# Performance work log

Hardware: AMD Instinct MI355X
Metric: run time of the kernel (lower is better)

Reference implementation:

```python
import jax, jax.numpy as jnp
import numpy as np

N = 50000   # nodes
E = 640000  # edges
IN_C, HID_C, OUT_C = 128, 128, 64


def _glorot(key, shape):
    lim = float(np.sqrt(6.0 / (shape[0] + shape[1])))
    return jax.random.uniform(key, shape, jnp.float32, -lim, lim)


def setup_inputs() -> dict:
    key = jax.random.key(0)
    ks = jax.random.split(key, 6)
    x = jax.random.normal(ks[0], (N, IN_C), jnp.float32)
    edge_index = jax.random.randint(ks[1], (2, E), 0, N, dtype=jnp.int64)
    W1 = _glorot(ks[2], (IN_C, HID_C));  b1 = jnp.zeros((HID_C,), jnp.float32)
    W2 = _glorot(ks[3], (HID_C, HID_C)); b2 = jnp.zeros((HID_C,), jnp.float32)
    W3 = _glorot(ks[4], (HID_C, OUT_C)); b3 = jnp.zeros((OUT_C,), jnp.float32)
    return {"x": x, "edge_index": edge_index,
            "W1": W1, "b1": b1, "W2": W2, "b2": b2, "W3": W3, "b3": b3}


def gcn_conv(x, W, b, src, dst, n_nodes):
    """PyG GCNConv (eval): add self-loops, D^-1/2 (A+I) D^-1/2, linear, bias."""
    h = x @ W  # [N, out]
    ones = jnp.ones(src.shape[0], h.dtype)
    # degree including the self-loop (+1 per node)
    deg = jax.ops.segment_sum(ones, dst, num_segments=n_nodes) + 1.0
    dinv_sqrt = jax.lax.rsqrt(deg)
    coef = dinv_sqrt[src] * dinv_sqrt[dst]               # [E]
    agg = jax.ops.segment_sum(h[src] * coef[:, None], dst, num_segments=n_nodes)
    agg = agg + h * (1.0 / deg)[:, None]                 # self-loop term: 1/deg[i]
    return agg + b


def reference(x, edge_index, W1, b1, W2, b2, W3, b3):
    src, dst = edge_index[0], edge_index[1]
    h = jax.nn.relu(gcn_conv(x, W1, b1, src, dst, N))
    h = jax.nn.relu(gcn_conv(h, W2, b2, src, dst, N))
    return gcn_conv(h, W3, b3, src, dst, N)
```

## Files before the change

kernel.cpp:

```cpp
#include <hip/hip_runtime.h>


#define K_DIM 128
#define POISON 0xAAAAAAAAu

typedef __attribute__((ext_vector_type(8))) short bf16x8;
typedef __attribute__((ext_vector_type(4))) float f32x4;

__device__ __forceinline__ unsigned short f2bf(float x) {
    unsigned u = __float_as_uint(x);
    return (unsigned short)((u + 0x7fffu + ((u >> 16) & 1u)) >> 16);
}
__device__ __forceinline__ float bflo(unsigned v) { return __uint_as_float(v << 16); }
__device__ __forceinline__ float bfhi(unsigned v) { return __uint_as_float(v & 0xffff0000u); }

__device__ __forceinline__ void add8(float* acc, uint4 v) {
    acc[0] += bflo(v.x); acc[1] += bfhi(v.x);
    acc[2] += bflo(v.y); acc[3] += bfhi(v.y);
    acc[4] += bflo(v.z); acc[5] += bfhi(v.z);
    acc[6] += bflo(v.w); acc[7] += bfhi(v.w);
}

template <int COUT>
__device__ __forceinline__ void gemm_tile_f32(const float* __restrict__ X,
                                              const unsigned short* __restrict__ Wt,
                                              const float* __restrict__ rsd,
                                              unsigned short* __restrict__ Hb,
                                              int nrows, int tile, int tid) {
    constexpr int NT = COUT / 16;
    const int wave = tid >> 6;
    const int lane = tid & 63;
    const int m16 = lane & 15;
    const int kg  = lane >> 4;
    const int r0w = tile * 64 + wave * 16;

    int arow = r0w + m16;
    if (arow >= nrows) arow = nrows - 1;

    bf16x8 a[4];
#pragma unroll
    for (int kb = 0; kb < 4; ++kb) {
        const float* xp = &X[(size_t)arow * 128 + kb * 32 + kg * 8];
        float4 v0 = *(const float4*)xp;
        float4 v1 = *(const float4*)(xp + 4);
        union { bf16x8 v; unsigned short u[8]; } ua;
        ua.u[0] = f2bf(v0.x); ua.u[1] = f2bf(v0.y);
        ua.u[2] = f2bf(v0.z); ua.u[3] = f2bf(v0.w);
        ua.u[4] = f2bf(v1.x); ua.u[5] = f2bf(v1.y);
        ua.u[6] = f2bf(v1.z); ua.u[7] = f2bf(v1.w);
        a[kb] = ua.v;
    }

    f32x4 acc[NT];
#pragma unroll
    for (int t = 0; t < NT; ++t) acc[t] = (f32x4){0.f, 0.f, 0.f, 0.f};

#pragma unroll
    for (int t = 0; t < NT; ++t) {
        const unsigned short* wp = &Wt[(size_t)(t * 16 + m16) * 128 + kg * 8];
#pragma unroll
        for (int kb = 0; kb < 4; ++kb) {
            bf16x8 b = *(const bf16x8*)&wp[kb * 32];
            acc[t] = __builtin_amdgcn_mfma_f32_16x16x32_bf16(a[kb], b, acc[t], 0, 0, 0);
        }
    }

    const int rowb = r0w + kg * 4;
#pragma unroll
    for (int t = 0; t < NT; ++t) {
#pragma unroll
        for (int i = 0; i < 4; ++i) {
            int r = rowb + i;
            if (r < nrows)
                Hb[(size_t)r * COUT + t * 16 + m16] = f2bf(acc[t][i] * rsd[r]);
        }
    }
}

__global__ void k_count_cvt(const int* __restrict__ dst, int* __restrict__ cnt,
                            unsigned short* __restrict__ erank,
                            const float* __restrict__ W1, const float* __restrict__ W2,
                            const float* __restrict__ W3,
                            unsigned short* __restrict__ Wt1, unsigned short* __restrict__ Wt2,
                            unsigned short* __restrict__ Wt3,
                            int E, int gCount) {
    if ((int)blockIdx.x < gCount) {
        const int G = gCount * 256;
        const int g = blockIdx.x * 256 + threadIdx.x;
        int d[4], ev[4];
#pragma unroll
        for (int q = 0; q < 4; ++q) {
            int e = g + q * G;
            ev[q] = e;
            d[q] = (e < E) ? dst[e] : -1;
        }
#pragma unroll
        for (int q = 0; q < 4; ++q)
            if (d[q] >= 0) {
                unsigned old = (unsigned)atomicAdd(&cnt[d[q]], 1);
                erank[ev[q]] = (unsigned short)(old - POISON);
            }
        return;
    }
    int j = (blockIdx.x - gCount) * 256 + threadIdx.x;
    if (j < 16384) { int nn = j >> 7, k = j & 127; Wt1[nn * 128 + k] = f2bf(W1[k * 128 + nn]); return; }
    j -= 16384;
    if (j < 16384) { int nn = j >> 7, k = j & 127; Wt2[nn * 128 + k] = f2bf(W2[k * 128 + nn]); return; }
    j -= 16384;
    if (j < 8192)  { int nn = j >> 7, k = j & 127; Wt3[nn * 128 + k] = f2bf(W3[k * 64 + nn]); return; }
}

__global__ void k_scan_block(const int* __restrict__ cnt, int* __restrict__ rowptr,
                             int* __restrict__ bsum, float* __restrict__ rsd, int n) {
    __shared__ int s[256];
    int t = threadIdx.x;
    int i = blockIdx.x * 256 + t;
    int v = (i < n) ? (int)((unsigned)cnt[i] - POISON) : 0;
    if (i < n) rsd[i] = rsqrtf((float)v + 1.0f);
    s[t] = v;
    __syncthreads();
#pragma unroll
    for (int d = 1; d < 256; d <<= 1) {
        int u = (t >= d) ? s[t - d] : 0;
        __syncthreads();
        s[t] += u;
        __syncthreads();
    }
    if (i < n) rowptr[i] = s[t] - v;
    if (t == 255) bsum[blockIdx.x] = s[255];
}

__global__ void k_scan_add(const int* __restrict__ bsum, int* __restrict__ rowptr,
                           int n, int E, int nscan) {
    __shared__ int s[256];
    __shared__ int off;
    int t = threadIdx.x;
    int v = (t < nscan) ? bsum[t] : 0;
    s[t] = v;
    __syncthreads();
#pragma unroll
    for (int d = 1; d < 256; d <<= 1) {
        int u = (t >= d) ? s[t - d] : 0;
        __syncthreads();
        s[t] += u;
        __syncthreads();
    }
    if (t == (int)blockIdx.x) off = s[t] - v;
    __syncthreads();
    int i = blockIdx.x * 256 + t;
    if (i < n) rowptr[i] += off;
    if (i == 0) rowptr[n] = E;
}

__global__ __launch_bounds__(256)
void k_fill_gemm1(const int* __restrict__ src, const int* __restrict__ dst,
                  const unsigned short* __restrict__ erank,
                  const int* __restrict__ rowptr, int* __restrict__ col,
                  const float* __restrict__ x, const unsigned short* __restrict__ Wt1,
                  const float* __restrict__ rsd, unsigned short* __restrict__ Hb1,
                  int N, int E, int gFill) {
    if ((int)blockIdx.x < gFill) {
        const int G = gFill * 256;
        const int g = blockIdx.x * 256 + threadIdx.x;
        int d[4], sv[4], rk[4];
#pragma unroll
        for (int q = 0; q < 4; ++q) {
            int e = g + q * G;
            if (e < E) { d[q] = dst[e]; sv[q] = src[e]; rk[q] = erank[e]; }
            else d[q] = -1;
        }
        int base[4];
#pragma unroll
        for (int q = 0; q < 4; ++q)
            if (d[q] >= 0) base[q] = rowptr[d[q]];
#pragma unroll
        for (int q = 0; q < 4; ++q)
            if (d[q] >= 0) col[base[q] + rk[q]] = sv[q];
        return;
    }
    gemm_tile_f32<128>(x, Wt1, rsd, Hb1, N, blockIdx.x - gFill, threadIdx.x);
}

template <int COUT>
__launch_bounds__(256)
__global__ void k_agg_gemm(const unsigned short* __restrict__ Hin,
                           const int* __restrict__ rowptr, const int* __restrict__ col,
                           const float* __restrict__ rsd, const float* __restrict__ bias,
                           const unsigned short* __restrict__ Wt,
                           unsigned short* __restrict__ Hout, int n) {
    constexpr int NT = COUT / 32;
    __shared__ unsigned short As[32][136];
    const int tid = threadIdx.x;
    const int r0 = blockIdx.x * 32;

    {
        const int lr = tid >> 3;
        const int lc = (tid & 7) * 16;
        const int row = r0 + lr;
        const int rc = (row < n) ? row : (n - 1);

        float acc[16];
#pragma unroll
        for (int j = 0; j < 16; ++j) acc[j] = 0.0f;
        {
            const unsigned short* hp = &Hin[(size_t)rc * 128 + lc];
            add8(acc, *(const uint4*)hp);
            add8(acc + 8, *(const uint4*)(hp + 8));
        }
        int e = rowptr[rc], end = rowptr[rc + 1];
        for (; e + 3 < end; e += 4) {
            const unsigned short* p0 = &Hin[(size_t)col[e]     * 128 + lc];
            const unsigned short* p1 = &Hin[(size_t)col[e + 1] * 128 + lc];
            const unsigned short* p2 = &Hin[(size_t)col[e + 2] * 128 + lc];
            const unsigned short* p3 = &Hin[(size_t)col[e + 3] * 128 + lc];
            uint4 a0 = *(const uint4*)p0, a1 = *(const uint4*)(p0 + 8);
            uint4 b0 = *(const uint4*)p1, b1 = *(const uint4*)(p1 + 8);
            uint4 c0 = *(const uint4*)p2, c1 = *(const uint4*)(p2 + 8);
            uint4 d0 = *(const uint4*)p3, d1 = *(const uint4*)(p3 + 8);
            add8(acc, a0); add8(acc + 8, a1);
            add8(acc, b0); add8(acc + 8, b1);
            add8(acc, c0); add8(acc + 8, c1);
            add8(acc, d0); add8(acc + 8, d1);
        }
        for (; e < end; ++e) {
            const unsigned short* p0 = &Hin[(size_t)col[e] * 128 + lc];
            add8(acc, *(const uint4*)p0);
            add8(acc + 8, *(const uint4*)(p0 + 8));
        }

        const float rs = rsd[rc];
        float r[16];
#pragma unroll
        for (int q = 0; q < 4; ++q) {
            float4 bq = *(const float4*)&bias[lc + q * 4];
            r[q * 4 + 0] = fmaxf(bq.x + rs * acc[q * 4 + 0], 0.0f);
            r[q * 4 + 1] = fmaxf(bq.y + rs * acc[q * 4 + 1], 0.0f);
            r[q * 4 + 2] = fmaxf(bq.z + rs * acc[q * 4 + 2], 0.0f);
            r[q * 4 + 3] = fmaxf(bq.w + rs * acc[q * 4 + 3], 0.0f);
        }
        uint4 o0, o1;
        o0.x = (unsigned)f2bf(r[0])  | ((unsigned)f2bf(r[1])  << 16);
        o0.y = (unsigned)f2bf(r[2])  | ((unsigned)f2bf(r[3])  << 16);
        o0.z = (unsigned)f2bf(r[4])  | ((unsigned)f2bf(r[5])  << 16);
        o0.w = (unsigned)f2bf(r[6])  | ((unsigned)f2bf(r[7])  << 16);
        o1.x = (unsigned)f2bf(r[8])  | ((unsigned)f2bf(r[9])  << 16);
        o1.y = (unsigned)f2bf(r[10]) | ((unsigned)f2bf(r[11]) << 16);
        o1.z = (unsigned)f2bf(r[12]) | ((unsigned)f2bf(r[13]) << 16);
        o1.w = (unsigned)f2bf(r[14]) | ((unsigned)f2bf(r[15]) << 16);
        *(uint4*)&As[lr][lc] = o0;
        *(uint4*)&As[lr][lc + 8] = o1;
    }
    __syncthreads();

    const int wave = tid >> 6;
    const int lane = tid & 63;
    const int m16 = lane & 15;
    const int kg  = lane >> 4;
    const int rloc = (wave >> 1) * 16 + m16;
    const int cbase = (wave & 1) * (COUT / 2);

    bf16x8 a[4];
#pragma unroll
    for (int kb = 0; kb < 4; ++kb)
        a[kb] = *(const bf16x8*)&As[rloc][kb * 32 + kg * 8];

    f32x4 acc2[NT];
#pragma unroll
    for (int t = 0; t < NT; ++t) acc2[t] = (f32x4){0.f, 0.f, 0.f, 0.f};

#pragma unroll
    for (int t = 0; t < NT; ++t) {
        const unsigned short* wp = &Wt[(size_t)(cbase + t * 16 + m16) * 128 + kg * 8];
#pragma unroll
        for (int kb = 0; kb < 4; ++kb) {
            bf16x8 b = *(const bf16x8*)&wp[kb * 32];
            acc2[t] = __builtin_amdgcn_mfma_f32_16x16x32_bf16(a[kb], b, acc2[t], 0, 0, 0);
        }
    }

    const int rowb = r0 + (wave >> 1) * 16 + kg * 4;
#pragma unroll
    for (int t = 0; t < NT; ++t) {
#pragma unroll
        for (int i = 0; i < 4; ++i) {
            int r = rowb + i;
            if (r < n)
                Hout[(size_t)r * COUT + cbase + t * 16 + m16] = f2bf(acc2[t][i] * rsd[r]);
        }
    }
}

template <int C>
__launch_bounds__(256)
__global__ void k_agg_final(const unsigned short* __restrict__ Hb,
                            const int* __restrict__ rowptr, const int* __restrict__ col,
                            const float* __restrict__ rsd, const float* __restrict__ bias,
                            float* __restrict__ OUT, int n) {
    constexpr int TPN = C / 8;
    constexpr int NPB = 256 / TPN;
    const int node = blockIdx.x * NPB + threadIdx.x / TPN;
    const int c = (threadIdx.x % TPN) * 8;
    if (node >= n) return;

    float acc[8];
#pragma unroll
    for (int j = 0; j < 8; ++j) acc[j] = 0.0f;
    add8(acc, *(const uint4*)&Hb[(size_t)node * C + c]);

    int e = rowptr[node], end = rowptr[node + 1];
    for (; e + 3 < end; e += 4) {
        uint4 v0 = *(const uint4*)&Hb[(size_t)col[e]     * C + c];
        uint4 v1 = *(const uint4*)&Hb[(size_t)col[e + 1] * C + c];
        uint4 v2 = *(const uint4*)&Hb[(size_t)col[e + 2] * C + c];
        uint4 v3 = *(const uint4*)&Hb[(size_t)col[e + 3] * C + c];
        add8(acc, v0); add8(acc, v1); add8(acc, v2); add8(acc, v3);
    }
    for (; e < end; ++e)
        add8(acc, *(const uint4*)&Hb[(size_t)col[e] * C + c]);

    const float rs = rsd[node];
    const float4 b0 = *(const float4*)&bias[c];
    const float4 b1 = *(const float4*)&bias[c + 4];
    float* po = &OUT[(size_t)node * C + c];
    *(float4*)&po[0] = make_float4(b0.x + rs * acc[0], b0.y + rs * acc[1],
                                   b0.z + rs * acc[2], b0.w + rs * acc[3]);
    *(float4*)&po[4] = make_float4(b1.x + rs * acc[4], b1.y + rs * acc[5],
                                   b1.z + rs * acc[6], b1.w + rs * acc[7]);
}


extern "C" void kernel_launch(void* const* d_in, const int* in_sizes, int n_in,
                              void* d_out, int out_size, void* d_ws, size_t ws_size,
                              hipStream_t stream) {
    const float* x  = (const float*)d_in[0];
    const int*   ei = (const int*)d_in[1];
    const float* W1 = (const float*)d_in[2];
    const float* b1 = (const float*)d_in[3];
    const float* W2 = (const float*)d_in[4];
    const float* b2 = (const float*)d_in[5];
    const float* W3 = (const float*)d_in[6];
    const float* b3 = (const float*)d_in[7];

    const int N = in_sizes[0] / K_DIM;
    const int E = in_sizes[1] / 2;
    const int* srcv = ei;
    const int* dstv = ei + E;

    char* ws = (char*)d_ws;
    size_t off = 0;
    auto alloc = [&](size_t bytes) {
        char* p = ws + off;
        off += (bytes + 255) & ~(size_t)255;
        return p;
    };
    int*   cnt    = (int*)alloc((size_t)N * 4);
    int*   rowptr = (int*)alloc((size_t)(N + 1) * 4);
    int*   bsum   = (int*)alloc(256 * 4);
    float* rsd    = (float*)alloc((size_t)N * 4);
    int*   col    = (int*)alloc((size_t)E * 4);
    unsigned short* erank = (unsigned short*)alloc((size_t)E * 2);
    unsigned short* Wt1 = (unsigned short*)alloc(128 * 128 * 2);
    unsigned short* Wt2 = (unsigned short*)alloc(128 * 128 * 2);
    unsigned short* Wt3 = (unsigned short*)alloc(64 * 128 * 2);
    unsigned short* Hb1 = (unsigned short*)alloc((size_t)N * 128 * 2);
    unsigned short* Hb2 = (unsigned short*)alloc((size_t)N * 128 * 2);
    unsigned short* Hb3 = (unsigned short*)alloc((size_t)N * 64 * 2);
    float* out = (float*)d_out;

    const int gN     = (N + 255) / 256;
    const int gE4    = (E + 1023) / 1024;
    const int gW     = (16384 + 16384 + 8192 + 255) / 256;
    const int gTiles = (N + 63) / 64;
    const int gF     = (N + 31) / 32;

    k_count_cvt<<<gE4 + gW, 256, 0, stream>>>(dstv, cnt, erank, W1, W2, W3,
                                              Wt1, Wt2, Wt3, E, gE4);
    k_scan_block<<<gN, 256, 0, stream>>>(cnt, rowptr, bsum, rsd, N);
    k_scan_add<<<gN, 256, 0, stream>>>(bsum, rowptr, N, E, gN);
    k_fill_gemm1<<<gE4 + gTiles, 256, 0, stream>>>(srcv, dstv, erank, rowptr, col,
                                                   x, Wt1, rsd, Hb1, N, E, gE4);

    k_agg_gemm<128><<<gF, 256, 0, stream>>>(Hb1, rowptr, col, rsd, b1, Wt2, Hb2, N);
    k_agg_gemm<64><<<gF, 256, 0, stream>>>(Hb2, rowptr, col, rsd, b2, Wt3, Hb3, N);
    k_agg_final<64><<<gF, 256, 0, stream>>>(Hb3, rowptr, col, rsd, b3, out, N);
}
```

Baseline: 244.8 us.

## Fold scan-add kernel into consumers via per-block redundant offset scan

Removes the separate k_scan_add launch. Every block of the fill, aggregation and final kernels now re-scans the block sums into shared memory and adds the per-256-node offset to rowptr on the fly, with the last row's end taken as E. This saves one kernel launch and a pass over rowptr. In exchange, each block of four kernels pays a 256-wide shared-memory scan with many barriers before doing its work.

Result: no change. 243.7 us (-0.4%).

```diff
diff --git a/kernel.cpp b/kernel.cpp
--- a/kernel.cpp
+++ b/kernel.cpp
@@ -19,6 +19,25 @@
     acc[2] += bflo(v.y); acc[3] += bfhi(v.y);
     acc[4] += bflo(v.z); acc[5] += bfhi(v.z);
     acc[6] += bflo(v.w); acc[7] += bfhi(v.w);
+}
+
+__device__ __forceinline__ void scan_prologue(const int* __restrict__ bsum,
+                                              int* soff, int nscan) {
+    int t = threadIdx.x;
+    int v = (t < nscan) ? bsum[t] : 0;
+    soff[t] = v;
+    __syncthreads();
+#pragma unroll
+    for (int d = 1; d < 256; d <<= 1) {
+        int u = (t >= d) ? soff[t - d] : 0;
+        __syncthreads();
+        soff[t] += u;
+        __syncthreads();
+    }
+    int excl = soff[t] - v;
+    __syncthreads();
+    soff[t] = excl;
+    __syncthreads();
 }
 
 template <int COUT>
@@ -130,36 +149,17 @@
     if (t == 255) bsum[blockIdx.x] = s[255];
 }
 
-__global__ void k_scan_add(const int* __restrict__ bsum, int* __restrict__ rowptr,
-                           int n, int E, int nscan) {
-    __shared__ int s[256];
-    __shared__ int off;
-    int t = threadIdx.x;
-    int v = (t < nscan) ? bsum[t] : 0;
-    s[t] = v;
-    __syncthreads();
-#pragma unroll
-    for (int d = 1; d < 256; d <<= 1) {
-        int u = (t >= d) ? s[t - d] : 0;
-        __syncthreads();
-        s[t] += u;
-        __syncthreads();
-    }
-    if (t == (int)blockIdx.x) off = s[t] - v;
-    __syncthreads();
-    int i = blockIdx.x * 256 + t;
-    if (i < n) rowptr[i] += off;
-    if (i == 0) rowptr[n] = E;
-}
-
 __global__ __launch_bounds__(256)
 void k_fill_gemm1(const int* __restrict__ src, const int* __restrict__ dst,
                   const unsigned short* __restrict__ erank,
-                  const int* __restrict__ rowptr, int* __restrict__ col,
+                  const int* __restrict__ rowptr, const int* __restrict__ bsum,
+                  int* __restrict__ col,
                   const float* __restrict__ x, const unsigned short* __restrict__ Wt1,
                   const float* __restrict__ rsd, unsigned short* __restrict__ Hb1,
-                  int N, int E, int gFill) {
+                  int N, int E, int gFill, int nscan) {
+    __shared__ int soff[256];
     if ((int)blockIdx.x < gFill) {
+        scan_prologue(bsum, soff, nscan);
         const int G = gFill * 256;
         const int g = blockIdx.x * 256 + threadIdx.x;
         int d[4], sv[4], rk[4];
@@ -172,7 +172,7 @@
         int base[4];
 #pragma unroll
         for (int q = 0; q < 4; ++q)
-            if (d[q] >= 0) base[q] = rowptr[d[q]];
+            if (d[q] >= 0) base[q] = rowptr[d[q]] + soff[d[q] >> 8];
 #pragma unroll
         for (int q = 0; q < 4; ++q)
             if (d[q] >= 0) col[base[q] + rk[q]] = sv[q];
@@ -184,14 +184,18 @@
 template <int COUT>
 __launch_bounds__(256)
 __global__ void k_agg_gemm(const unsigned short* __restrict__ Hin,
-                           const int* __restrict__ rowptr, const int* __restrict__ col,
+                           const int* __restrict__ rowptr, const int* __restrict__ bsum,
+                           const int* __restrict__ col,
                            const float* __restrict__ rsd, const float* __restrict__ bias,
                            const unsigned short* __restrict__ Wt,
-                           unsigned short* __restrict__ Hout, int n) {
+                           unsigned short* __restrict__ Hout, int n, int E, int nscan) {
     constexpr int NT = COUT / 32;
     __shared__ unsigned short As[32][136];
+    __shared__ int soff[256];
     const int tid = threadIdx.x;
     const int r0 = blockIdx.x * 32;
+
+    scan_prologue(bsum, soff, nscan);
 
     {
         const int lr = tid >> 3;
@@ -207,7 +211,8 @@
             add8(acc, *(const uint4*)hp);
             add8(acc + 8, *(const uint4*)(hp + 8));
         }
-        int e = rowptr[rc], end = rowptr[rc + 1];
+        int e = rowptr[rc] + soff[rc >> 8];
+        int end = (rc + 1 == n) ? E : rowptr[rc + 1] + soff[(rc + 1) >> 8];
         for (; e + 3 < end; e += 4) {
             const unsigned short* p0 = &Hin[(size_t)col[e]     * 128 + lc];
             const unsigned short* p1 = &Hin[(size_t)col[e + 1] * 128 + lc];
@@ -293,11 +298,15 @@
 template <int C>
 __launch_bounds__(256)
 __global__ void k_agg_final(const unsigned short* __restrict__ Hb,
-                            const int* __restrict__ rowptr, const int* __restrict__ col,
+                            const int* __restrict__ rowptr, const int* __restrict__ bsum,
+                            const int* __restrict__ col,
                             const float* __restrict__ rsd, const float* __restrict__ bias,
-                            float* __restrict__ OUT, int n) {
+                            float* __restrict__ OUT, int n, int E, int nscan) {
     constexpr int TPN = C / 8;
     constexpr int NPB = 256 / TPN;
+    __shared__ int soff[256];
+    scan_prologue(bsum, soff, nscan);
+
     const int node = blockIdx.x * NPB + threadIdx.x / TPN;
     const int c = (threadIdx.x % TPN) * 8;
     if (node >= n) return;
@@ -307,7 +316,8 @@
     for (int j = 0; j < 8; ++j) acc[j] = 0.0f;
     add8(acc, *(const uint4*)&Hb[(size_t)node * C + c]);
 
-    int e = rowptr[node], end = rowptr[node + 1];
+    int e = rowptr[node] + soff[node >> 8];
+    int end = (node + 1 == n) ? E : rowptr[node + 1] + soff[(node + 1) >> 8];
     for (; e + 3 < end; e += 4) {
         uint4 v0 = *(const uint4*)&Hb[(size_t)col[e]     * C + c];
         uint4 v1 = *(const uint4*)&Hb[(size_t)col[e + 1] * C + c];
@@ -376,11 +386,10 @@
     k_count_cvt<<<gE4 + gW, 256, 0, stream>>>(dstv, cnt, erank, W1, W2, W3,
                                               Wt1, Wt2, Wt3, E, gE4);
     k_scan_block<<<gN, 256, 0, stream>>>(cnt, rowptr, bsum, rsd, N);
-    k_scan_add<<<gN, 256, 0, stream>>>(bsum, rowptr, N, E, gN);
-    k_fill_gemm1<<<gE4 + gTiles, 256, 0, stream>>>(srcv, dstv, erank, rowptr, col,
-                                                   x, Wt1, rsd, Hb1, N, E, gE4);
-
-    k_agg_gemm<128><<<gF, 256, 0, stream>>>(Hb1, rowptr, col, rsd, b1, Wt2, Hb2, N);
-    k_agg_gemm<64><<<gF, 256, 0, stream>>>(Hb2, rowptr, col, rsd, b2, Wt3, Hb3, N);
-    k_agg_final<64><<<gF, 256, 0, stream>>>(Hb3, rowptr, col, rsd, b3, out, N);
-}
+    k_fill_gemm1<<<gE4 + gTiles, 256, 0, stream>>>(srcv, dstv, erank, rowptr, bsum, col,
+                                                   x, Wt1, rsd, Hb1, N, E, gE4, gN);
+
+    k_agg_gemm<128><<<gF, 256, 0, stream>>>(Hb1, rowptr, bsum, col, rsd, b1, Wt2, Hb2, N, E, gN);
+    k_agg_gemm<64><<<gF, 256, 0, stream>>>(Hb2, rowptr, bsum, col, rsd, b2, Wt3, Hb3, N, E, gN);
+    k_agg_final<64><<<gF, 256, 0, stream>>>(Hb3, rowptr, bsum, col, rsd, b3, out, N, E, gN);
+}
```
